# Kernel tuning notes

Measured on AMD Instinct MI355X. Metric: run time of the kernel, lower is better.

The kernel has to match this reference:

```python
import jax, jax.numpy as jnp
import numpy as np

B, T, D, H, FA = 512, 64, 128, 128, 64


def setup_inputs() -> dict:
    key = jax.random.key(0)
    ks = jax.random.split(key, 14)
    n = lambda k, s: jax.random.normal(k, s, dtype=jnp.float32) * 0.05
    return {
        "X": jax.random.normal(ks[0], (B, T, D), dtype=jnp.float32),
        "attri_data": jax.random.normal(ks[1], (D, FA), dtype=jnp.float32),
        "w_attr1": n(ks[2], (FA, FA // 2)), "b_attr1": n(ks[3], (FA // 2,)),
        "w_attr2": n(ks[4], (FA // 2, 1)), "b_attr2": n(ks[5], (1,)),
        "w_a1": n(ks[6], (2 * H + T, H)), "b_a1": n(ks[7], (H,)),
        "w_a2": n(ks[8], (H, 1)), "b_a2": n(ks[9], (1,)),
        "w_ih": n(ks[10], (4 * H, D)), "w_hh": n(ks[11], (4 * H, H)),
        "b_ih": n(ks[12], (4 * H,)), "b_hh": n(ks[13], (4 * H,)),
    }


def reference(X, attri_data, w_attr1, b_attr1, w_attr2, b_attr2,
              w_a1, b_a1, w_a2, b_a2, w_ih, w_hh, b_ih, b_hh):
    b, t_dim, d = X.shape
    h_dim = w_hh.shape[1]

    # Attribute attention: softmax over the data_dim axis (dim=0)
    a = attri_data @ w_attr1 + b_attr1
    a = jnp.where(a > 0, a, 0.5 * a)  # LeakyReLU(negative_slope=0.5)
    alpha_attri = jax.nn.softmax(a @ w_attr2 + b_attr2, axis=0)  # [D, 1]
    X_attri = X * alpha_attri.reshape(1, 1, d)  # [B, T, D]
    Xp = jnp.transpose(X_attri, (0, 2, 1))      # [B, D, T] per-variable series

    def step(carry, x_t):  # x_t: [B, D]
        h, c = carry  # [B, H] each; state BEFORE consuming x_t (matches torch loop)
        feat = jnp.concatenate([
            jnp.broadcast_to(h[:, None, :], (b, d, h_dim)),
            jnp.broadcast_to(c[:, None, :], (b, d, h_dim)),
            Xp,
        ], axis=2)  # [B, D, 2H+T]
        e = jnp.tanh(feat @ w_a1 + b_a1) @ w_a2 + b_a2  # [B, D, 1]
        alpha_s = jax.nn.softmax(e[..., 0], axis=1)      # softmax over D
        x_tilde_t = alpha_s * x_t                        # [B, D]
        # LSTM cell (PyTorch gate order i, f, g, o)
        gates = x_t @ w_ih.T + b_ih + h @ w_hh.T + b_hh  # [B, 4H]
        i_g, f_g, g_g, o_g = jnp.split(gates, 4, axis=1)
        c_new = jax.nn.sigmoid(f_g) * c + jax.nn.sigmoid(i_g) * jnp.tanh(g_g)
        h_new = jax.nn.sigmoid(o_g) * jnp.tanh(c_new)
        return (h_new, c_new), x_tilde_t

    h0 = jnp.zeros((b, h_dim), X.dtype)
    c0 = jnp.zeros((b, h_dim), X.dtype)
    _, X_tilde = jax.lax.scan(step, (h0, c0), jnp.transpose(X_attri, (1, 0, 2)))
    return jnp.transpose(X_tilde, (1, 0, 2))  # [B, T, D]
```

## Files before the change

### kernel.cpp

```cpp
#include <hip/hip_runtime.h>
#include <hip/hip_bf16.h>
#include <cstddef>
#include <cstdint>

#define DEVI __device__ __forceinline__

typedef float f32x4 __attribute__((ext_vector_type(4)));
typedef __bf16 bf16x8 __attribute__((ext_vector_type(8)));

DEVI float fast_rcp(float x) { return __builtin_amdgcn_rcpf(x); }
DEVI float sigmoid_fast(float x) { return fast_rcp(1.0f + __expf(-x)); }
DEVI float tanh_fast(float x) { return 1.0f - 2.0f * fast_rcp(__expf(2.0f * x) + 1.0f); }
DEVI float4 ld4(const float* p) { return *reinterpret_cast<const float4*>(p); }
DEVI void st4(float* p, float4 v) { *reinterpret_cast<float4*>(p) = v; }
DEVI float f4c(const float4& v, int i) { return i == 0 ? v.x : i == 1 ? v.y : i == 2 ? v.z : v.w; }
DEVI unsigned short bfbits(float f) { return __builtin_bit_cast(unsigned short, (__bf16)f); }
DEVI unsigned pack2(float a, float b) {
  return (unsigned)bfbits(a) | ((unsigned)bfbits(b) << 16);
}

__global__ __launch_bounds__(128) void k_alpha(
    const float* __restrict__ AD, const float* __restrict__ W1,
    const float* __restrict__ B1, const float* __restrict__ W2,
    const float* __restrict__ B2, float* __restrict__ alpha) {
  __shared__ float sW1[64 * 32];
  __shared__ float sW2[32];
  __shared__ float sB1[32];
  __shared__ float red[128];
  __shared__ float s_mx, s_sum;
  int tid = threadIdx.x;
  for (int i = tid; i < 64 * 32; i += 128) sW1[i] = W1[i];
  if (tid < 32) { sW2[tid] = W2[tid]; sB1[tid] = B1[tid]; }
  __syncthreads();
  float ad[64];
  #pragma unroll
  for (int f = 0; f < 64; ++f) ad[f] = AD[tid * 64 + f];
  float logit = B2[0];
  #pragma unroll
  for (int j = 0; j < 32; ++j) {
    float a = sB1[j];
    #pragma unroll
    for (int f = 0; f < 64; ++f) a = fmaf(ad[f], sW1[f * 32 + j], a);
    a = a > 0.0f ? a : 0.5f * a;
    logit = fmaf(a, sW2[j], logit);
  }
  red[tid] = logit;
  __syncthreads();
  if (tid == 0) {
    float mx = red[0];
    for (int i = 1; i < 128; ++i) mx = fmaxf(mx, red[i]);
    float sm = 0.0f;
    for (int i = 0; i < 128; ++i) sm += __expf(red[i] - mx);
    s_mx = mx; s_sum = sm;
  }
  __syncthreads();
  alpha[tid] = __expf(logit - s_mx) / s_sum;
}

__global__ __launch_bounds__(256) void k_tw(
    const float* __restrict__ w_a1, __hip_bfloat16* __restrict__ w1T) {
  __shared__ float tile[64][132];
  int blk = blockIdx.x;
  int tid = threadIdx.x;
  #pragma unroll
  for (int i = 0; i < 32; ++i) {
    int idx = i * 256 + tid;
    int r = idx >> 7, c = idx & 127;
    tile[r][c] = w_a1[(size_t)(blk * 64 + r) * 128 + c];
  }
  __syncthreads();
  int n = tid >> 1, mh = tid & 1;
  unsigned* dst = reinterpret_cast<unsigned*>(&w1T[(size_t)n * 256 + blk * 64 + mh * 32]);
  #pragma unroll
  for (int i = 0; i < 16; ++i) {
    float a = tile[mh * 32 + 2 * i][n];
    float b = tile[mh * 32 + 2 * i + 1][n];
    dst[i] = pack2(a, b);
  }
}

__global__ __launch_bounds__(256) void k_ep(
    const float* __restrict__ X, const float* __restrict__ w_a1,
    const float* __restrict__ b_a1, const float* __restrict__ alpha,
    float* __restrict__ EP) {
  __shared__ float Xb[64][128];
  __shared__ float Wx[64][128];
  int b = blockIdx.x;
  int tid = threadIdx.x;
  #pragma unroll
  for (int i = 0; i < 8; ++i) {
    int l4 = i * 256 + tid;
    int r = l4 >> 5, c4 = l4 & 31;
    st4(&Xb[r][c4 * 4], ld4(&X[((size_t)b * 64 + r) * 128 + c4 * 4]));
    st4(&Wx[r][c4 * 4], ld4(&w_a1[(size_t)(256 + r) * 128 + c4 * 4]));
  }
  __syncthreads();
  int dg = tid & 15, kg = tid >> 4;
  float acc[8][8] = {};
  #pragma unroll 4
  for (int tau = 0; tau < 64; ++tau) {
    float4 xa0 = ld4(&Xb[tau][dg * 4]);
    float4 xa1 = ld4(&Xb[tau][64 + dg * 4]);
    float4 wa0 = ld4(&Wx[tau][kg * 4]);
    float4 wa1 = ld4(&Wx[tau][64 + kg * 4]);
    #pragma unroll
    for (int i = 0; i < 8; ++i) {
      float xv = (i < 4) ? f4c(xa0, i) : f4c(xa1, i - 4);
      #pragma unroll
      for (int j = 0; j < 4; ++j) {
        acc[i][j]     = fmaf(xv, f4c(wa0, j), acc[i][j]);
        acc[i][j + 4] = fmaf(xv, f4c(wa1, j), acc[i][j + 4]);
      }
    }
  }
  float4 ba0 = ld4(&b_a1[kg * 4]);
  float4 ba1v = ld4(&b_a1[64 + kg * 4]);
  #pragma unroll
  for (int i = 0; i < 8; ++i) {
    int drow = (i < 4) ? dg * 4 + i : 64 + dg * 4 + (i - 4);
    float al = alpha[drow];
    float4 o0, o1;
    float* p0 = &o0.x; float* p1 = &o1.x;
    #pragma unroll
    for (int j = 0; j < 4; ++j) {
      float v0 = 2.0f * fmaf(al, acc[i][j],     f4c(ba0, j));
      float v1 = 2.0f * fmaf(al, acc[i][j + 4], f4c(ba1v, j));
      p0[j] = __expf(fminf(fmaxf(v0, -40.0f), 40.0f));
      p1[j] = __expf(fminf(fmaxf(v1, -40.0f), 40.0f));
    }
    st4(&EP[((size_t)b * 128 + drow) * 128 + kg * 4], o0);
    st4(&EP[((size_t)b * 128 + drow) * 128 + 64 + kg * 4], o1);
  }
}

__global__ __launch_bounds__(512, 1) void k_rec(
    const float* __restrict__ X, const float* __restrict__ w_ih,
    const float* __restrict__ w_hh, const float* __restrict__ b_ih,
    const float* __restrict__ b_hh, const float* __restrict__ alpha,
    __hip_bfloat16* __restrict__ S) {
  __shared__ unsigned short kB[2][16 * 256];
  int tid = threadIdx.x;
  int wv = tid >> 6, l = tid & 63, lg = l >> 4, lr = l & 15;
  int b0 = blockIdx.x * 16;

  bf16x8 afr[8][4];
  #pragma unroll
  for (int ks = 0; ks < 8; ++ks) {
    int kb = (ks & 3) * 32 + lg * 8;
    float4 a0, a1;
    if (ks < 4) { a0 = ld4(&alpha[kb]); a1 = ld4(&alpha[kb + 4]); }
    #pragma unroll
    for (int q = 0; q < 4; ++q) {
      int j = q * 128 + wv * 16 + lr;
      const float* src = (ks < 4) ? &w_ih[(size_t)j * 128 + kb]
                                  : &w_hh[(size_t)j * 128 + kb];
      float4 f0 = ld4(src), f1 = ld4(src + 4);
      if (ks < 4) {
        f0.x *= a0.x; f0.y *= a0.y; f0.z *= a0.z; f0.w *= a0.w;
        f1.x *= a1.x; f1.y *= a1.y; f1.z *= a1.z; f1.w *= a1.w;
      }
      bf16x8 fr;
      fr[0] = (__bf16)f0.x; fr[1] = (__bf16)f0.y;
      fr[2] = (__bf16)f0.z; fr[3] = (__bf16)f0.w;
      fr[4] = (__bf16)f1.x; fr[5] = (__bf16)f1.y;
      fr[6] = (__bf16)f1.z; fr[7] = (__bf16)f1.w;
      afr[ks][q] = fr;
    }
  }

  float bias[4][4];
  #pragma unroll
  for (int q = 0; q < 4; ++q)
    #pragma unroll
    for (int r = 0; r < 4; ++r) {
      int j = q * 128 + wv * 16 + lg * 4 + r;
      bias[q][r] = b_ih[j] + b_hh[j];
    }

  alignas(16) float hA[4] = {0.f, 0.f, 0.f, 0.f};
  alignas(16) float cA[4] = {0.f, 0.f, 0.f, 0.f};

  int bi = tid >> 5, d0 = (tid & 31) * 4;
  int m0 = wv * 16 + lg * 4;
  int k0 = 128 + m0;
  int xoff = bi * 256 + (((d0 >> 3) ^ (bi & 7)) << 3) + (d0 & 7);
  int hoff = lr * 256 + (((k0 >> 3) ^ (lr & 7)) << 3) + (k0 & 7);

  const float* xbase = &X[(size_t)(b0 + bi) * 64 * 128 + d0];

  {
    float4 x0 = ld4(xbase);
    uint2 xu; xu.x = pack2(x0.x, x0.y); xu.y = pack2(x0.z, x0.w);
    *reinterpret_cast<uint2*>(&kB[0][xoff]) = xu;
    uint2 z; z.x = 0u; z.y = 0u;
    *reinterpret_cast<uint2*>(&kB[0][hoff]) = z;
  }
  float4 xa = ld4(xbase + 1 * 128);
  float4 xb = ld4(xbase + 2 * 128);
  __syncthreads();

  for (int t = 0; t < 64; ++t) {
    int cur = t & 1, nxt = cur ^ 1;

    bf16x8 bfr[8];
    #pragma unroll
    for (int ks = 0; ks < 8; ++ks) {
      int kb = ks * 32 + lg * 8;
      int idx = lr * 256 + (((kb >> 3) ^ (lr & 7)) << 3) + (kb & 7);
      bfr[ks] = *reinterpret_cast<const bf16x8*>(&kB[cur][idx]);
    }

    int tn = (t + 3 < 64) ? t + 3 : 63;
    float4 xc = ld4(xbase + (size_t)tn * 128);

    size_t srow = ((size_t)(t * 512) + b0 + lr) * 256;
    uint2 hS; hS.x = pack2(hA[0], hA[1]); hS.y = pack2(hA[2], hA[3]);
    uint2 cS; cS.x = pack2(cA[0], cA[1]); cS.y = pack2(cA[2], cA[3]);
    *reinterpret_cast<uint2*>(&S[srow + m0]) = hS;
    *reinterpret_cast<uint2*>(&S[srow + 128 + m0]) = cS;

    f32x4 aX[4], aH[4];
    #pragma unroll
    for (int q = 0; q < 4; ++q) { aX[q] = (f32x4){0.f,0.f,0.f,0.f}; aH[q] = (f32x4){0.f,0.f,0.f,0.f}; }
    #pragma unroll
    for (int ks = 0; ks < 4; ++ks) {
      #pragma unroll
      for (int q = 0; q < 4; ++q)
        aX[q] = __builtin_amdgcn_mfma_f32_16x16x32_bf16(afr[ks][q], bfr[ks], aX[q], 0, 0, 0);
      #pragma unroll
      for (int q = 0; q < 4; ++q)
        aH[q] = __builtin_amdgcn_mfma_f32_16x16x32_bf16(afr[ks + 4][q], bfr[ks + 4], aH[q], 0, 0, 0);
    }

    #pragma unroll
    for (int r = 0; r < 4; ++r) {
      float g0 = aX[0][r] + aH[0][r] + bias[0][r];
      float g1 = aX[1][r] + aH[1][r] + bias[1][r];
      float g2 = aX[2][r] + aH[2][r] + bias[2][r];
      float g3 = aX[3][r] + aH[3][r] + bias[3][r];
      float ig = sigmoid_fast(g0);
      float fg = sigmoid_fast(g1);
      float gg = tanh_fast(g2);
      float og = sigmoid_fast(g3);
      float cn = fmaf(fg, cA[r], ig * gg);
      float hn = og * tanh_fast(cn);
      cA[r] = cn;
      hA[r] = hn;
    }

    uint2 xu; xu.x = pack2(xa.x, xa.y); xu.y = pack2(xa.z, xa.w);
    *reinterpret_cast<uint2*>(&kB[nxt][xoff]) = xu;
    uint2 hu; hu.x = pack2(hA[0], hA[1]); hu.y = pack2(hA[2], hA[3]);
    *reinterpret_cast<uint2*>(&kB[nxt][hoff]) = hu;
    xa = xb; xb = xc;
    __syncthreads();
  }
}

__global__ __launch_bounds__(256, 1) void k_eq(
    const __hip_bfloat16* __restrict__ S, const __hip_bfloat16* __restrict__ w1T,
    float* __restrict__ EQ) {
  int tid = threadIdx.x;
  int wv = tid >> 6, l = tid & 63;
  int lr = l & 15, lg = l >> 4;
  int r0 = blockIdx.x * 128 + wv * 32;

  bf16x8 a[2][8];
  #pragma unroll
  for (int ri = 0; ri < 2; ++ri)
    #pragma unroll
    for (int ks = 0; ks < 8; ++ks)
      a[ri][ks] = *reinterpret_cast<const bf16x8*>(
          &S[(size_t)(r0 + ri * 16 + lr) * 256 + ks * 32 + lg * 8]);

  f32x4 acc[2][8];
  #pragma unroll
  for (int ri = 0; ri < 2; ++ri)
    #pragma unroll
    for (int nj = 0; nj < 8; ++nj) acc[ri][nj] = (f32x4){0.f, 0.f, 0.f, 0.f};

  #pragma unroll
  for (int nj = 0; nj < 8; ++nj) {
    bf16x8 bf[8];
    #pragma unroll
    for (int ks = 0; ks < 8; ++ks)
      bf[ks] = *reinterpret_cast<const bf16x8*>(
          &w1T[(size_t)(nj * 16 + lr) * 256 + ks * 32 + lg * 8]);
    #pragma unroll
    for (int ks = 0; ks < 8; ++ks) {
      acc[0][nj] = __builtin_amdgcn_mfma_f32_16x16x32_bf16(a[0][ks], bf[ks], acc[0][nj], 0, 0, 0);
      acc[1][nj] = __builtin_amdgcn_mfma_f32_16x16x32_bf16(a[1][ks], bf[ks], acc[1][nj], 0, 0, 0);
    }
  }

  #pragma unroll
  for (int ri = 0; ri < 2; ++ri)
    #pragma unroll
    for (int nj = 0; nj < 8; ++nj)
      #pragma unroll
      for (int r = 0; r < 4; ++r) {
        int grow = r0 + ri * 16 + lg * 4 + r;
        int n = nj * 16 + lr;
        float v = 2.0f * acc[ri][nj][r];
        EQ[(size_t)grow * 128 + n] = __expf(fminf(fmaxf(v, -40.f), 40.f));
      }
}

__global__ __launch_bounds__(512, 2) void k_attn(
    const float* __restrict__ EP, const float* __restrict__ EQ,
    const float* __restrict__ w_a2, const float* __restrict__ alpha,
    const float* __restrict__ X, float* __restrict__ out) {
  __shared__ float EQs[64][128];
  __shared__ float e_lds[8][128];
  int b = blockIdx.x;
  int tid = threadIdx.x;
  #pragma unroll
  for (int i = 0; i < 4; ++i) {
    int l4 = i * 512 + tid;
    int t = l4 >> 5, k4 = l4 & 31;
    st4(&EQs[t][k4 * 4], ld4(&EQ[((size_t)t * 512 + b) * 128 + k4 * 4]));
  }
  int d = tid >> 2, s = tid & 3;
  float4 ep[8], w2r[8];
  #pragma unroll
  for (int q = 0; q < 8; ++q) {
    ep[q]  = ld4(&EP[((size_t)b * 128 + d) * 128 + s * 32 + q * 4]);
    w2r[q] = ld4(&w_a2[s * 32 + q * 4]);
  }
  int wv = tid >> 6, l = tid & 63;
  float al0 = alpha[l], al1 = alpha[64 + l];
  __syncthreads();

  for (int rnd = 0; rnd < 8; ++rnd) {
    #pragma unroll
    for (int it = 0; it < 8; ++it) {
      int t = rnd * 8 + it;
      float p = 0.0f;
      #pragma unroll
      for (int q = 0; q < 8; ++q) {
        float4 eq = ld4(&EQs[t][s * 32 + q * 4]);
        p = fmaf(w2r[q].x, fast_rcp(fmaf(ep[q].x, eq.x, 1.0f)), p);
        p = fmaf(w2r[q].y, fast_rcp(fmaf(ep[q].y, eq.y, 1.0f)), p);
        p = fmaf(w2r[q].z, fast_rcp(fmaf(ep[q].z, eq.z, 1.0f)), p);
        p = fmaf(w2r[q].w, fast_rcp(fmaf(ep[q].w, eq.w, 1.0f)), p);
      }
      p += __shfl_xor(p, 1);
      p += __shfl_xor(p, 2);
      if (s == 0) e_lds[it][d] = -2.0f * p;
    }
    __syncthreads();
    {
      int t = rnd * 8 + wv;
      float v0 = e_lds[wv][l], v1 = e_lds[wv][64 + l];
      float mx = fmaxf(v0, v1);
      #pragma unroll
      for (int o = 1; o < 64; o <<= 1) mx = fmaxf(mx, __shfl_xor(mx, o));
      float e0 = __expf(v0 - mx), e1 = __expf(v1 - mx);
      float sm = e0 + e1;
      #pragma unroll
      for (int o = 1; o < 64; o <<= 1) sm += __shfl_xor(sm, o);
      float inv = fast_rcp(sm);
      size_t ro = ((size_t)b * 64 + t) * 128;
      out[ro + l]      = e0 * inv * al0 * X[ro + l];
      out[ro + 64 + l] = e1 * inv * al1 * X[ro + 64 + l];
    }
    __syncthreads();
  }
}

extern "C" void kernel_launch(void* const* d_in, const int* in_sizes, int n_in,
                              void* d_out, int out_size, void* d_ws, size_t ws_size,
                              hipStream_t stream) {
  const float* X    = (const float*)d_in[0];
  const float* AD   = (const float*)d_in[1];
  const float* W1   = (const float*)d_in[2];
  const float* B1   = (const float*)d_in[3];
  const float* W2   = (const float*)d_in[4];
  const float* B2   = (const float*)d_in[5];
  const float* w_a1 = (const float*)d_in[6];
  const float* b_a1 = (const float*)d_in[7];
  const float* w_a2 = (const float*)d_in[8];
  const float* w_ih = (const float*)d_in[10];
  const float* w_hh = (const float*)d_in[11];
  const float* b_ih = (const float*)d_in[12];
  const float* b_hh = (const float*)d_in[13];
  float* out = (float*)d_out;
  float* ws = (float*)d_ws;

  float* alpha = ws;
  float* EQ    = ws + 256;
  float* EP    = EQ + 4194304;
  __hip_bfloat16* S   = (__hip_bfloat16*)(EP + 8388608);
  __hip_bfloat16* w1T = (__hip_bfloat16*)(EP + 8388608 + 4194304);

  hipLaunchKernelGGL(k_alpha, dim3(1),   dim3(128), 0, stream, AD, W1, B1, W2, B2, alpha);
  hipLaunchKernelGGL(k_tw,    dim3(4),   dim3(256), 0, stream, w_a1, w1T);
  hipLaunchKernelGGL(k_ep,    dim3(512), dim3(256), 0, stream, X, w_a1, b_a1, alpha, EP);
  hipLaunchKernelGGL(k_rec,   dim3(32),  dim3(512), 0, stream, X, w_ih, w_hh, b_ih, b_hh, alpha, S);
  hipLaunchKernelGGL(k_eq,    dim3(256), dim3(256), 0, stream, S, w1T, EQ);
  hipLaunchKernelGGL(k_attn,  dim3(512), dim3(512), 0, stream, EP, EQ, w_a2, alpha, X, out);
}
```

Before: 305.9 us.

## Hoist LSTM input projection out of recurrence into parallel GEMM kernel

```diff
diff --git a/kernel.cpp b/kernel.cpp
--- a/kernel.cpp
+++ b/kernel.cpp
@@ -18,6 +18,20 @@
 DEVI unsigned pack2(float a, float b) {
   return (unsigned)bfbits(a) | ((unsigned)bfbits(b) << 16);
 }
+DEVI f32x4 cvt4(uint2 u) {
+  f32x4 r;
+  r[0] = __builtin_bit_cast(float, (u.x & 0xffffu) << 16);
+  r[1] = __builtin_bit_cast(float, u.x & 0xffff0000u);
+  r[2] = __builtin_bit_cast(float, (u.y & 0xffffu) << 16);
+  r[3] = __builtin_bit_cast(float, u.y & 0xffff0000u);
+  return r;
+}
+DEVI void barrier_lgkm() {
+  __builtin_amdgcn_sched_barrier(0);
+  asm volatile("s_waitcnt lgkmcnt(0)" ::: "memory");
+  __builtin_amdgcn_s_barrier();
+  __builtin_amdgcn_sched_barrier(0);
+}
 
 __global__ __launch_bounds__(128) void k_alpha(
     const float* __restrict__ AD, const float* __restrict__ W1,
@@ -57,6 +71,26 @@
   alpha[tid] = __expf(logit - s_mx) / s_sum;
 }
 
+__global__ __launch_bounds__(256) void k_wih(
+    const float* __restrict__ w_ih, const float* __restrict__ alpha,
+    const float* __restrict__ b_ih, const float* __restrict__ b_hh,
+    __hip_bfloat16* __restrict__ wA, float* __restrict__ biasJ) {
+  int i4 = blockIdx.x * 256 + threadIdx.x;
+  int j = i4 >> 5, d0 = (i4 & 31) * 4;
+  float4 w = ld4(&w_ih[(size_t)j * 128 + d0]);
+  float4 a = ld4(&alpha[d0]);
+  uint2 o;
+  o.x = pack2(w.x * a.x, w.y * a.y);
+  o.y = pack2(w.z * a.z, w.w * a.w);
+  *reinterpret_cast<uint2*>(&wA[(size_t)j * 128 + d0]) = o;
+  if (i4 < 128) {
+    int jb = i4 * 4;
+    float4 v0 = ld4(&b_ih[jb]), v1 = ld4(&b_hh[jb]);
+    v0.x += v1.x; v0.y += v1.y; v0.z += v1.z; v0.w += v1.w;
+    st4(&biasJ[jb], v0);
+  }
+}
+
 __global__ __launch_bounds__(256) void k_tw(
     const float* __restrict__ w_a1, __hip_bfloat16* __restrict__ w1T) {
   __shared__ float tile[64][132];
@@ -133,128 +167,153 @@
   }
 }
 
-__global__ __launch_bounds__(512, 1) void k_rec(
-    const float* __restrict__ X, const float* __restrict__ w_ih,
-    const float* __restrict__ w_hh, const float* __restrict__ b_ih,
-    const float* __restrict__ b_hh, const float* __restrict__ alpha,
-    __hip_bfloat16* __restrict__ S) {
-  __shared__ unsigned short kB[2][16 * 256];
+__global__ __launch_bounds__(256, 2) void k_gxw(
+    const float* __restrict__ X, const __hip_bfloat16* __restrict__ wA,
+    const float* __restrict__ biasJ, __hip_bfloat16* __restrict__ gx) {
+  int rt = blockIdx.x, jt = blockIdx.y;
   int tid = threadIdx.x;
   int wv = tid >> 6, l = tid & 63, lg = l >> 4, lr = l & 15;
-  int b0 = blockIdx.x * 16;
-
-  bf16x8 afr[8][4];
-  #pragma unroll
-  for (int ks = 0; ks < 8; ++ks) {
-    int kb = (ks & 3) * 32 + lg * 8;
-    float4 a0, a1;
-    if (ks < 4) { a0 = ld4(&alpha[kb]); a1 = ld4(&alpha[kb + 4]); }
-    #pragma unroll
-    for (int q = 0; q < 4; ++q) {
-      int j = q * 128 + wv * 16 + lr;
-      const float* src = (ks < 4) ? &w_ih[(size_t)j * 128 + kb]
-                                  : &w_hh[(size_t)j * 128 + kb];
+  int r0 = rt * 128;
+  int j0 = jt * 128 + wv * 32;
+
+  bf16x8 a[2][4];
+  #pragma unroll
+  for (int ri = 0; ri < 2; ++ri)
+    #pragma unroll
+    for (int ks = 0; ks < 4; ++ks)
+      a[ri][ks] = *reinterpret_cast<const bf16x8*>(
+          &wA[(size_t)(j0 + ri * 16 + lr) * 128 + ks * 32 + lg * 8]);
+
+  f32x4 acc[2][8];
+  #pragma unroll
+  for (int ri = 0; ri < 2; ++ri)
+    #pragma unroll
+    for (int nj = 0; nj < 8; ++nj) acc[ri][nj] = (f32x4){0.f, 0.f, 0.f, 0.f};
+
+  #pragma unroll 2
+  for (int nj = 0; nj < 8; ++nj) {
+    bf16x8 bh[4];
+    #pragma unroll
+    for (int ks = 0; ks < 4; ++ks) {
+      const float* src = &X[(size_t)(r0 + nj * 16 + lr) * 128 + ks * 32 + lg * 8];
       float4 f0 = ld4(src), f1 = ld4(src + 4);
-      if (ks < 4) {
-        f0.x *= a0.x; f0.y *= a0.y; f0.z *= a0.z; f0.w *= a0.w;
-        f1.x *= a1.x; f1.y *= a1.y; f1.z *= a1.z; f1.w *= a1.w;
-      }
       bf16x8 fr;
       fr[0] = (__bf16)f0.x; fr[1] = (__bf16)f0.y;
       fr[2] = (__bf16)f0.z; fr[3] = (__bf16)f0.w;
       fr[4] = (__bf16)f1.x; fr[5] = (__bf16)f1.y;
       fr[6] = (__bf16)f1.z; fr[7] = (__bf16)f1.w;
-      afr[ks][q] = fr;
-    }
-  }
-
-  float bias[4][4];
-  #pragma unroll
-  for (int q = 0; q < 4; ++q)
-    #pragma unroll
-    for (int r = 0; r < 4; ++r) {
-      int j = q * 128 + wv * 16 + lg * 4 + r;
-      bias[q][r] = b_ih[j] + b_hh[j];
+      bh[ks] = fr;
+    }
+    #pragma unroll
+    for (int ks = 0; ks < 4; ++ks) {
+      acc[0][nj] = __builtin_amdgcn_mfma_f32_16x16x32_bf16(a[0][ks], bh[ks], acc[0][nj], 0, 0, 0);
+      acc[1][nj] = __builtin_amdgcn_mfma_f32_16x16x32_bf16(a[1][ks], bh[ks], acc[1][nj], 0, 0, 0);
+    }
+  }
+
+  #pragma unroll
+  for (int ri = 0; ri < 2; ++ri) {
+    int jb = j0 + ri * 16 + lg * 4;
+    float4 bi = ld4(&biasJ[jb]);
+    #pragma unroll
+    for (int nj = 0; nj < 8; ++nj) {
+      int row = r0 + nj * 16 + lr;
+      uint2 o;
+      o.x = pack2(acc[ri][nj][0] + bi.x, acc[ri][nj][1] + bi.y);
+      o.y = pack2(acc[ri][nj][2] + bi.z, acc[ri][nj][3] + bi.w);
+      *reinterpret_cast<uint2*>(&gx[(size_t)row * 512 + jb]) = o;
+    }
+  }
+}
+
+__global__ __launch_bounds__(512, 1) void k_rec(
+    const __hip_bfloat16* __restrict__ gx, const float* __restrict__ w_hh,
+    __hip_bfloat16* __restrict__ S) {
+  __shared__ unsigned short kB[2][16 * 128];
+  int tid = threadIdx.x;
+  int wv = tid >> 6, l = tid & 63, lg = l >> 4, lr = l & 15;
+  int b0 = blockIdx.x * 16;
+
+  bf16x8 ah[4][4];
+  #pragma unroll
+  for (int ks = 0; ks < 4; ++ks)
+    #pragma unroll
+    for (int q = 0; q < 4; ++q) {
+      const float* src = &w_hh[(size_t)(q * 128 + wv * 16 + lr) * 128 + ks * 32 + lg * 8];
+      float4 f0 = ld4(src), f1 = ld4(src + 4);
+      bf16x8 fr;
+      fr[0] = (__bf16)f0.x; fr[1] = (__bf16)f0.y;
+      fr[2] = (__bf16)f0.z; fr[3] = (__bf16)f0.w;
+      fr[4] = (__bf16)f1.x; fr[5] = (__bf16)f1.y;
+      fr[6] = (__bf16)f1.z; fr[7] = (__bf16)f1.w;
+      ah[ks][q] = fr;
     }
 
   alignas(16) float hA[4] = {0.f, 0.f, 0.f, 0.f};
   alignas(16) float cA[4] = {0.f, 0.f, 0.f, 0.f};
-
-  int bi = tid >> 5, d0 = (tid & 31) * 4;
   int m0 = wv * 16 + lg * 4;
-  int k0 = 128 + m0;
-  int xoff = bi * 256 + (((d0 >> 3) ^ (bi & 7)) << 3) + (d0 & 7);
-  int hoff = lr * 256 + (((k0 >> 3) ^ (lr & 7)) << 3) + (k0 & 7);
-
-  const float* xbase = &X[(size_t)(b0 + bi) * 64 * 128 + d0];
-
-  {
-    float4 x0 = ld4(xbase);
-    uint2 xu; xu.x = pack2(x0.x, x0.y); xu.y = pack2(x0.z, x0.w);
-    *reinterpret_cast<uint2*>(&kB[0][xoff]) = xu;
-    uint2 z; z.x = 0u; z.y = 0u;
-    *reinterpret_cast<uint2*>(&kB[0][hoff]) = z;
-  }
-  float4 xa = ld4(xbase + 1 * 128);
-  float4 xb = ld4(xbase + 2 * 128);
-  __syncthreads();
-
-  for (int t = 0; t < 64; ++t) {
-    int cur = t & 1, nxt = cur ^ 1;
-
-    bf16x8 bfr[8];
-    #pragma unroll
-    for (int ks = 0; ks < 8; ++ks) {
-      int kb = ks * 32 + lg * 8;
-      int idx = lr * 256 + (((kb >> 3) ^ (lr & 7)) << 3) + (kb & 7);
-      bfr[ks] = *reinterpret_cast<const bf16x8*>(&kB[cur][idx]);
-    }
-
-    int tn = (t + 3 < 64) ? t + 3 : 63;
-    float4 xc = ld4(xbase + (size_t)tn * 128);
-
-    size_t srow = ((size_t)(t * 512) + b0 + lr) * 256;
-    uint2 hS; hS.x = pack2(hA[0], hA[1]); hS.y = pack2(hA[2], hA[3]);
-    uint2 cS; cS.x = pack2(cA[0], cA[1]); cS.y = pack2(cA[2], cA[3]);
-    *reinterpret_cast<uint2*>(&S[srow + m0]) = hS;
-    *reinterpret_cast<uint2*>(&S[srow + 128 + m0]) = cS;
-
-    f32x4 aX[4], aH[4];
-    #pragma unroll
-    for (int q = 0; q < 4; ++q) { aX[q] = (f32x4){0.f,0.f,0.f,0.f}; aH[q] = (f32x4){0.f,0.f,0.f,0.f}; }
-    #pragma unroll
-    for (int ks = 0; ks < 4; ++ks) {
-      #pragma unroll
-      for (int q = 0; q < 4; ++q)
-        aX[q] = __builtin_amdgcn_mfma_f32_16x16x32_bf16(afr[ks][q], bfr[ks], aX[q], 0, 0, 0);
-      #pragma unroll
-      for (int q = 0; q < 4; ++q)
-        aH[q] = __builtin_amdgcn_mfma_f32_16x16x32_bf16(afr[ks + 4][q], bfr[ks + 4], aH[q], 0, 0, 0);
-    }
-
-    #pragma unroll
-    for (int r = 0; r < 4; ++r) {
-      float g0 = aX[0][r] + aH[0][r] + bias[0][r];
-      float g1 = aX[1][r] + aH[1][r] + bias[1][r];
-      float g2 = aX[2][r] + aH[2][r] + bias[2][r];
-      float g3 = aX[3][r] + aH[3][r] + bias[3][r];
-      float ig = sigmoid_fast(g0);
-      float fg = sigmoid_fast(g1);
-      float gg = tanh_fast(g2);
-      float og = sigmoid_fast(g3);
-      float cn = fmaf(fg, cA[r], ig * gg);
-      float hn = og * tanh_fast(cn);
-      cA[r] = cn;
-      hA[r] = hn;
-    }
-
-    uint2 xu; xu.x = pack2(xa.x, xa.y); xu.y = pack2(xa.z, xa.w);
-    *reinterpret_cast<uint2*>(&kB[nxt][xoff]) = xu;
-    uint2 hu; hu.x = pack2(hA[0], hA[1]); hu.y = pack2(hA[2], hA[3]);
-    *reinterpret_cast<uint2*>(&kB[nxt][hoff]) = hu;
-    xa = xb; xb = xc;
-    __syncthreads();
-  }
+  int wIdx = lr * 128 + (((m0 >> 3) ^ lr) << 3) + (m0 & 7);
+  const __hip_bfloat16* gxb = gx + (size_t)(b0 + lr) * 64 * 512 + wv * 16 + lg * 4;
+
+  uint2 z; z.x = 0u; z.y = 0u;
+  *reinterpret_cast<uint2*>(&kB[0][wIdx]) = z;
+  uint2 gA[4], gB[4];
+  #pragma unroll
+  for (int q = 0; q < 4; ++q) gA[q] = *reinterpret_cast<const uint2*>(gxb + q * 128);
+  #pragma unroll
+  for (int q = 0; q < 4; ++q) gB[q] = *reinterpret_cast<const uint2*>(gxb + 512 + q * 128);
+  __syncthreads();
+
+#define REC_STEP(T, SRC, DST, G)                                               \
+  do {                                                                         \
+    int t_ = (T);                                                              \
+    bf16x8 bh[4];                                                              \
+    _Pragma("unroll")                                                          \
+    for (int ks = 0; ks < 4; ++ks)                                             \
+      bh[ks] = *reinterpret_cast<const bf16x8*>(                               \
+          &kB[SRC][lr * 128 + ((((ks << 2) + lg) ^ lr) << 3)]);                \
+    f32x4 ac0 = cvt4(G[0]), ac1 = cvt4(G[1]), ac2 = cvt4(G[2]), ac3 = cvt4(G[3]); \
+    int tn_ = t_ + 2 < 64 ? t_ + 2 : 63;                                       \
+    _Pragma("unroll")                                                          \
+    for (int q = 0; q < 4; ++q)                                                \
+      G[q] = *reinterpret_cast<const uint2*>(gxb + (size_t)tn_ * 512 + q * 128); \
+    {                                                                          \
+      uint2 hS; hS.x = pack2(hA[0], hA[1]); hS.y = pack2(hA[2], hA[3]);        \
+      uint2 cS; cS.x = pack2(cA[0], cA[1]); cS.y = pack2(cA[2], cA[3]);        \
+      __hip_bfloat16* sp = S + ((size_t)(t_ * 512) + b0 + lr) * 256 + m0;      \
+      *reinterpret_cast<uint2*>(sp) = hS;                                      \
+      *reinterpret_cast<uint2*>(sp + 128) = cS;                                \
+    }                                                                          \
+    _Pragma("unroll")                                                          \
+    for (int ks = 0; ks < 4; ++ks) {                                           \
+      ac0 = __builtin_amdgcn_mfma_f32_16x16x32_bf16(ah[ks][0], bh[ks], ac0, 0, 0, 0); \
+      ac1 = __builtin_amdgcn_mfma_f32_16x16x32_bf16(ah[ks][1], bh[ks], ac1, 0, 0, 0); \
+      ac2 = __builtin_amdgcn_mfma_f32_16x16x32_bf16(ah[ks][2], bh[ks], ac2, 0, 0, 0); \
+      ac3 = __builtin_amdgcn_mfma_f32_16x16x32_bf16(ah[ks][3], bh[ks], ac3, 0, 0, 0); \
+    }                                                                          \
+    _Pragma("unroll")                                                          \
+    for (int r = 0; r < 4; ++r) {                                              \
+      float ig = sigmoid_fast(ac0[r]);                                         \
+      float fg = sigmoid_fast(ac1[r]);                                         \
+      float gg = tanh_fast(ac2[r]);                                            \
+      float og = sigmoid_fast(ac3[r]);                                         \
+      float cn = fmaf(fg, cA[r], ig * gg);                                     \
+      float hn = og * tanh_fast(cn);                                           \
+      cA[r] = cn; hA[r] = hn;                                                  \
+    }                                                                          \
+    {                                                                          \
+      uint2 hu; hu.x = pack2(hA[0], hA[1]); hu.y = pack2(hA[2], hA[3]);        \
+      *reinterpret_cast<uint2*>(&kB[DST][wIdx]) = hu;                          \
+    }                                                                          \
+    barrier_lgkm();                                                            \
+  } while (0)
+
+  #pragma unroll 1
+  for (int it = 0; it < 32; ++it) {
+    REC_STEP(2 * it, 0, 1, gA);
+    REC_STEP(2 * it + 1, 1, 0, gB);
+  }
+#undef REC_STEP
 }
 
 __global__ __launch_bounds__(256, 1) void k_eq(
@@ -329,7 +388,7 @@
   }
   int wv = tid >> 6, l = tid & 63;
   float al0 = alpha[l], al1 = alpha[64 + l];
-  __syncthreads();
+  barrier_lgkm();
 
   for (int rnd = 0; rnd < 8; ++rnd) {
     #pragma unroll
@@ -348,7 +407,7 @@
       p += __shfl_xor(p, 2);
       if (s == 0) e_lds[it][d] = -2.0f * p;
     }
-    __syncthreads();
+    barrier_lgkm();
     {
       int t = rnd * 8 + wv;
       float v0 = e_lds[wv][l], v1 = e_lds[wv][64 + l];
@@ -364,7 +423,7 @@
       out[ro + l]      = e0 * inv * al0 * X[ro + l];
       out[ro + 64 + l] = e1 * inv * al1 * X[ro + 64 + l];
     }
-    __syncthreads();
+    barrier_lgkm();
   }
 }
 
@@ -390,13 +449,22 @@
   float* alpha = ws;
   float* EQ    = ws + 256;
   float* EP    = EQ + 4194304;
-  __hip_bfloat16* S   = (__hip_bfloat16*)(EP + 8388608);
-  __hip_bfloat16* w1T = (__hip_bfloat16*)(EP + 8388608 + 4194304);
+  float* fS    = EP + 8388608;
+  __hip_bfloat16* S = (__hip_bfloat16*)fS;
+  float* fgx   = fS + 4194304;
+  __hip_bfloat16* gx = (__hip_bfloat16*)fgx;
+  float* fw1T  = fgx + 8388608;
+  __hip_bfloat16* w1T = (__hip_bfloat16*)fw1T;
+  float* fwA   = fw1T + 16384;
+  __hip_bfloat16* wA = (__hip_bfloat16*)fwA;
+  float* biasJ = fwA + 32768;
 
   hipLaunchKernelGGL(k_alpha, dim3(1),   dim3(128), 0, stream, AD, W1, B1, W2, B2, alpha);
+  hipLaunchKernelGGL(k_wih,   dim3(64),  dim3(256), 0, stream, w_ih, alpha, b_ih, b_hh, wA, biasJ);
   hipLaunchKernelGGL(k_tw,    dim3(4),   dim3(256), 0, stream, w_a1, w1T);
   hipLaunchKernelGGL(k_ep,    dim3(512), dim3(256), 0, stream, X, w_a1, b_a1, alpha, EP);
-  hipLaunchKernelGGL(k_rec,   dim3(32),  dim3(512), 0, stream, X, w_ih, w_hh, b_ih, b_hh, alpha, S);
+  hipLaunchKernelGGL(k_gxw,   dim3(256, 4), dim3(256), 0, stream, X, wA, biasJ, gx);
+  hipLaunchKernelGGL(k_rec,   dim3(32),  dim3(512), 0, stream, gx, w_hh, S);
   hipLaunchKernelGGL(k_eq,    dim3(256), dim3(256), 0, stream, S, w1T, EQ);
   hipLaunchKernelGGL(k_attn,  dim3(512), dim3(512), 0, stream, EP, EQ, w_a2, alpha, X, out);
 }
```

Measured after the change: 362.9 us. 18.6% more time.
